# Performance work log

Hardware: AMD Instinct MI355X
Metric: run time of the kernel (lower is better)

The kernel has to match this reference:

```python
import jax, jax.numpy as jnp
import numpy as np

N, K, D = 131072, 64, 256


def setup_inputs() -> dict:
    key = jax.random.key(0)
    k1, k2, k3, k4, k5 = jax.random.split(key, 5)
    X = jax.random.normal(k1, (N, D), dtype=jnp.float32)
    # mixture weights: positive, sum to 1 (log is taken)
    weights = jax.nn.softmax(jax.random.normal(k2, (K,), dtype=jnp.float32))
    means = jax.random.normal(k3, (K, D), dtype=jnp.float32)
    # precision Cholesky factors: lower-triangular with positive diagonal
    tril = jnp.tril(0.01 * jax.random.normal(k4, (K, D, D), dtype=jnp.float32), k=-1)
    diag = 0.5 + jax.random.uniform(k5, (K, D), dtype=jnp.float32)  # in (0.5, 1.5)
    precision_cholesky = tril + jax.vmap(jnp.diag)(diag)
    return {"X": X, "weights": weights, "means": means,
            "precision_cholesky": precision_cholesky}


def reference(X, weights, means, precision_cholesky):
    n_samples, n_features = X.shape
    # log|L_k| = sum of log of diagonal entries (sklearn's strided-diagonal trick)
    log_det = jnp.sum(jnp.log(jnp.diagonal(precision_cholesky, axis1=1, axis2=2)), axis=1)  # (K,)

    # Per-component Mahalanobis distance, sequential over K to avoid an [N,K,D] buffer
    def mahalanobis(args):
        mu, prec_chol = args                      # (D,), (D,D)
        y = X @ prec_chol - mu @ prec_chol        # (N,D)
        return jnp.sum(y * y, axis=1)             # (N,)

    sq = jax.lax.map(mahalanobis, (means, precision_cholesky))  # (K,N)

    log_prob = -0.5 * (n_features * jnp.log(2.0 * jnp.pi) + sq.T) + log_det  # (N,K)
    weighted_log_prob = log_prob + jnp.log(weights)                          # (N,K)
    log_prob_norm = jax.nn.logsumexp(weighted_log_prob, axis=1)              # (N,)
    log_resp = weighted_log_prob - log_prob_norm[:, None]                    # (N,K)
    return jnp.mean(log_prob_norm), log_resp
```

## Files before the change

### kernel.cpp

```cpp
#include <hip/hip_runtime.h>
#include <hip/hip_bf16.h>
#include <cmath>


typedef unsigned short ushort_t;
typedef __attribute__((ext_vector_type(4))) float f32x4;
typedef __attribute__((ext_vector_type(8))) short bf16x8;

constexpr int N_ = 131072;
constexpr int K_ = 64;
constexpr int D_ = 256;
constexpr int BM = 128;
constexpr int NBLK = N_ / BM;
constexpr int SQLD = 68;

__device__ __forceinline__ ushort_t f2bf(float v) {
  unsigned u = __float_as_uint(v);
  u += 0x7FFFu + ((u >> 16) & 1u);
  return (ushort_t)(u >> 16);
}

__device__ __forceinline__ void gld16(const ushort_t* g, ushort_t* l) {
  __builtin_amdgcn_global_load_lds(
      (const __attribute__((address_space(1))) unsigned int*)g,
      (__attribute__((address_space(3))) unsigned int*)l, 16, 0, 0);
}

__device__ __forceinline__ float dpp_red16(float v) {
  int x = __float_as_int(v);
  v += __int_as_float(__builtin_amdgcn_update_dpp(0, x, 0xB1, 0xF, 0xF, true));
  x = __float_as_int(v);
  v += __int_as_float(__builtin_amdgcn_update_dpp(0, x, 0x4E, 0xF, 0xF, true));
  x = __float_as_int(v);
  v += __int_as_float(__builtin_amdgcn_update_dpp(0, x, 0x141, 0xF, 0xF, true));
  x = __float_as_int(v);
  v += __int_as_float(__builtin_amdgcn_update_dpp(0, x, 0x140, 0xF, 0xF, true));
  return v;
}

__global__ void prep_x(const float* __restrict__ X, ushort_t* __restrict__ Xb) {
  for (int e = blockIdx.x * blockDim.x + threadIdx.x; e < N_ * D_;
       e += gridDim.x * blockDim.x) {
    int j = e & 7;
    int lane = (e >> 3) & 63;
    int kc = (e >> 9) & 7;
    int mm = (e >> 12) & 7;
    int T = e >> 15;
    int row = T * 128 + mm * 16 + (lane & 15);
    int col = kc * 32 + (lane >> 4) * 8 + j;
    Xb[e] = f2bf(X[(size_t)row * D_ + col]);
  }
}

__global__ void prep_p(const float* __restrict__ P, ushort_t* __restrict__ Pb) {
  for (int e = blockIdx.x * blockDim.x + threadIdx.x; e < K_ * D_ * D_;
       e += gridDim.x * blockDim.x) {
    int j = e & 7;
    int lane = (e >> 3) & 63;
    int n = (e >> 9) & 3;
    int wc = (e >> 11) & 3;
    int g = e >> 13;
    int k = g >> 3, s = g & 7;
    int row_p = s * 32 + (lane >> 4) * 8 + j;
    int col_p = wc * 64 + n * 16 + (lane & 15);
    Pb[e] = f2bf(P[((size_t)k * D_ + row_p) * D_ + col_p]);
  }
}

__global__ void prep_t(const float* __restrict__ P, const float* __restrict__ mu,
                       const float* __restrict__ w, ushort_t* __restrict__ tvb,
                       float* __restrict__ C) {
  int k = blockIdx.x, j = threadIdx.x;
  const float* Pk = P + (size_t)k * D_ * D_;
  const float* muk = mu + (size_t)k * D_;
  float acc = 0.f;
  for (int i = 0; i < D_; ++i) acc += muk[i] * Pk[(size_t)i * D_ + j];
  tvb[k * D_ + j] = f2bf(acc);
  __shared__ float red[D_];
  red[j] = logf(Pk[(size_t)j * D_ + j]);
  __syncthreads();
  for (int s = 128; s > 0; s >>= 1) {
    if (j < s) red[j] += red[j + s];
    __syncthreads();
  }
  if (j == 0)
    C[k] = red[0] + logf(w[k]) - 0.5f * (float)D_ * logf(2.0f * (float)M_PI);
}

__global__ __launch_bounds__(512, 2) void gmm_main(
    const ushort_t* __restrict__ Xb, const ushort_t* __restrict__ Pb,
    const ushort_t* __restrict__ tvb,
    float* __restrict__ wlp ) {
  __shared__ __align__(16) ushort_t Bl[4][8192];
  __shared__ __align__(16) ushort_t tvl[16384];
  __shared__ float sqf[BM * SQLD];

  const int tid = threadIdx.x;
  const int T = blockIdx.x;
  const int lane = tid & 63, wid = tid >> 6;
  const int wr = wid >> 2, wc = wid & 3;
  const int lc = lane & 15, lg = lane >> 4;

#pragma unroll
  for (int i = 0; i < 17; ++i) sqf[tid + i * 512] = 0.f;

  const ushort_t* Ag = Xb + (size_t)T * 32768;
  bf16x8 Areg[32];
#pragma unroll
  for (int m = 0; m < 4; ++m)
#pragma unroll
    for (int c = 0; c < 8; ++c)
      Areg[m * 8 + c] =
          *(const bf16x8*)&Ag[(((wr * 4 + m) * 8 + c) * 512) + lane * 8];

#pragma unroll
  for (int it = 0; it < 4; ++it)
    gld16(tvb + (it * 512 + tid) * 8, &tvl[(it * 512 + tid) * 8]);
#pragma unroll
  for (int it = 0; it < 2; ++it)
    gld16(Pb + (it * 512 + tid) * 8, &Bl[0][(it * 512 + tid) * 8]);
#pragma unroll
  for (int it = 0; it < 2; ++it)
    gld16(Pb + 8192 + (it * 512 + tid) * 8, &Bl[1][(it * 512 + tid) * 8]);

  asm volatile("s_waitcnt vmcnt(0) lgkmcnt(0)" ::: "memory");
  __builtin_amdgcn_s_barrier();

#pragma unroll 1
  for (int k = 0; k < K_; ++k) {
    f32x4 acc[4][4];
#pragma unroll
    for (int m = 0; m < 4; ++m)
#pragma unroll
      for (int n = 0; n < 4; ++n) acc[m][n] = (f32x4){0.f, 0.f, 0.f, 0.f};

#pragma unroll
    for (int s = 0; s < 8; ++s) {
      const int g2 = k * 8 + s + 2;
      const ushort_t* gb = Pb + (size_t)g2 * 8192;
      ushort_t* db = &Bl[(s + 2) & 3][0];
#pragma unroll
      for (int it = 0; it < 2; ++it)
        gld16(gb + (it * 512 + tid) * 8, db + (it * 512 + tid) * 8);
      asm volatile("s_waitcnt vmcnt(4)" ::: "memory");
      __builtin_amdgcn_s_barrier();

      bf16x8 bb[4];
#pragma unroll
      for (int n = 0; n < 4; ++n)
        bb[n] = *(const bf16x8*)&Bl[s & 3][(wc * 4 + n) * 512 + lane * 8];
#pragma unroll
      for (int m = 0; m < 4; ++m)
#pragma unroll
        for (int n = 0; n < 4; ++n)
          acc[m][n] = __builtin_amdgcn_mfma_f32_16x16x32_bf16(
              Areg[m * 8 + s], bb[n], acc[m][n], 0, 0, 0);
    }

    float tv[4];
#pragma unroll
    for (int n = 0; n < 4; ++n) {
      ushort_t uv = tvl[k * 256 + wc * 64 + n * 16 + lc];
      tv[n] = __uint_as_float((unsigned)uv << 16);
    }
#pragma unroll
    for (int m = 0; m < 4; ++m)
#pragma unroll
      for (int r = 0; r < 4; ++r) {
        float d0 = acc[m][0][r] - tv[0];
        float d1 = acc[m][1][r] - tv[1];
        float d2 = acc[m][2][r] - tv[2];
        float d3 = acc[m][3][r] - tv[3];
        float sfl = dpp_red16(d0 * d0 + d1 * d1 + d2 * d2 + d3 * d3);
        if (lc == 0) {
          int row = wr * 64 + m * 16 + lg * 4 + r;
          atomicAdd(&sqf[row * SQLD + k], sfl);
        }
      }
  }

  __syncthreads();

  float* dst = wlp + (size_t)T * BM * K_;
#pragma unroll
  for (int i = 0; i < 4; ++i) {
    int idx4 = tid + i * 512;
    int row = idx4 >> 4, c4 = idx4 & 15;
    ((f32x4*)dst)[idx4] = *(const f32x4*)&sqf[row * SQLD + c4 * 4];
  }
}

__global__ void lse_k(float* __restrict__ out, const float* __restrict__ C,
                      float* __restrict__ partial) {
  const int row = blockIdx.x * 256 + threadIdx.x;
  float* w = out + 1 + (size_t)row * K_;
  float v[K_];
  float mx = -1e30f;
#pragma unroll
  for (int j = 0; j < K_; ++j) {
    v[j] = -0.5f * w[j] + C[j];
    mx = fmaxf(mx, v[j]);
  }
  float ssum = 0.f;
#pragma unroll
  for (int j = 0; j < K_; ++j) ssum += expf(v[j] - mx);
  float l = mx + logf(ssum);
#pragma unroll
  for (int j = 0; j < K_; ++j) w[j] = v[j] - l;
  __shared__ float red[256];
  red[threadIdx.x] = l;
  __syncthreads();
  for (int s = 128; s > 0; s >>= 1) {
    if (threadIdx.x < s) red[threadIdx.x] += red[threadIdx.x + s];
    __syncthreads();
  }
  if (threadIdx.x == 0) partial[blockIdx.x] = red[0];
}

__global__ void final_red(const float* __restrict__ partial,
                          float* __restrict__ out) {
  __shared__ float red[512];
  red[threadIdx.x] = partial[threadIdx.x];
  __syncthreads();
  for (int s = 256; s > 0; s >>= 1) {
    if (threadIdx.x < s) red[threadIdx.x] += red[threadIdx.x + s];
    __syncthreads();
  }
  if (threadIdx.x == 0) out[0] = red[0] * (1.0f / (float)N_);
}

extern "C" void kernel_launch(void* const* d_in, const int* in_sizes, int n_in,
                              void* d_out, int out_size, void* d_ws,
                              size_t ws_size, hipStream_t stream) {
  const float* X = (const float*)d_in[0];
  const float* w = (const float*)d_in[1];
  const float* mu = (const float*)d_in[2];
  const float* P = (const float*)d_in[3];
  float* out = (float*)d_out;
  char* ws = (char*)d_ws;

  ushort_t* Xb = (ushort_t*)ws;
  ushort_t* Pb = (ushort_t*)(ws + 67108864);
  ushort_t* tvb = (ushort_t*)(ws + 75530240);
  float* C = (float*)(ws + 75563008);
  float* partial = (float*)(ws + 75563264);

  prep_x<<<2048, 256, 0, stream>>>(X, Xb);
  prep_p<<<2048, 256, 0, stream>>>(P, Pb);
  prep_t<<<K_, 256, 0, stream>>>(P, mu, w, tvb, C);
  gmm_main<<<NBLK, 512, 0, stream>>>(Xb, Pb, tvb, out + 1);
  lse_k<<<N_ / 256, 256, 0, stream>>>(out, C, partial);
  final_red<<<1, 512, 0, stream>>>(partial, out);
}
```

Measured before the change: 1.017 ms.

## Switch main GEMM to 32x32x16 MFMA tiles with matching operand layouts

Replaces the 16x16x32 bf16 MFMA tiling with 32x32x16 MFMA instructions. The X and P pre-permutation kernels and the per-wave register layout change to match. The epilogue reduction now covers 32-lane column groups, using a DPP reduction followed by a ds_swizzle across the two 16-lane halves. The intent is higher MFMA throughput and fewer LDS operand reads per FLOP. In exchange, each accumulator is larger and the lane-to-row mapping in the epilogue becomes more complex.

```diff
diff --git a/kernel.cpp b/kernel.cpp
--- a/kernel.cpp
+++ b/kernel.cpp
@@ -4,6 +4,7 @@
 
 
 typedef unsigned short ushort_t;
+typedef __attribute__((ext_vector_type(16))) float f32x16;
 typedef __attribute__((ext_vector_type(4))) float f32x4;
 typedef __attribute__((ext_vector_type(8))) short bf16x8;
 
@@ -42,12 +43,13 @@
   for (int e = blockIdx.x * blockDim.x + threadIdx.x; e < N_ * D_;
        e += gridDim.x * blockDim.x) {
     int j = e & 7;
-    int lane = (e >> 3) & 63;
-    int kc = (e >> 9) & 7;
-    int mm = (e >> 12) & 7;
+    int l = (e >> 3) & 63;
+    int mk = (e >> 9) & 31;
+    int wr = (e >> 14) & 1;
     int T = e >> 15;
-    int row = T * 128 + mm * 16 + (lane & 15);
-    int col = kc * 32 + (lane >> 4) * 8 + j;
+    int mt = mk & 1, ks = mk >> 1;
+    int row = T * 128 + wr * 64 + mt * 32 + (l & 31);
+    int col = ks * 16 + (l >> 5) * 8 + j;
     Xb[e] = f2bf(X[(size_t)row * D_ + col]);
   }
 }
@@ -57,12 +59,13 @@
        e += gridDim.x * blockDim.x) {
     int j = e & 7;
     int lane = (e >> 3) & 63;
-    int n = (e >> 9) & 3;
+    int kc = (e >> 9) & 1;
+    int n = (e >> 10) & 1;
     int wc = (e >> 11) & 3;
     int g = e >> 13;
     int k = g >> 3, s = g & 7;
-    int row_p = s * 32 + (lane >> 4) * 8 + j;
-    int col_p = wc * 64 + n * 16 + (lane & 15);
+    int row_p = s * 32 + kc * 16 + (lane >> 5) * 8 + j;
+    int col_p = wc * 64 + n * 32 + (lane & 31);
     Pb[e] = f2bf(P[((size_t)k * D_ + row_p) * D_ + col_p]);
   }
 }
@@ -99,19 +102,16 @@
   const int T = blockIdx.x;
   const int lane = tid & 63, wid = tid >> 6;
   const int wr = wid >> 2, wc = wid & 3;
-  const int lc = lane & 15, lg = lane >> 4;
+  const int l31 = lane & 31, lh = lane >> 5;
 
 #pragma unroll
   for (int i = 0; i < 17; ++i) sqf[tid + i * 512] = 0.f;
 
-  const ushort_t* Ag = Xb + (size_t)T * 32768;
+  const ushort_t* Ag = Xb + (size_t)(T * 2 + wr) * 16384;
   bf16x8 Areg[32];
 #pragma unroll
-  for (int m = 0; m < 4; ++m)
-#pragma unroll
-    for (int c = 0; c < 8; ++c)
-      Areg[m * 8 + c] =
-          *(const bf16x8*)&Ag[(((wr * 4 + m) * 8 + c) * 512) + lane * 8];
+  for (int f = 0; f < 32; ++f)
+    Areg[f] = *(const bf16x8*)&Ag[f * 512 + lane * 8];
 
 #pragma unroll
   for (int it = 0; it < 4; ++it)
@@ -128,11 +128,20 @@
 
 #pragma unroll 1
   for (int k = 0; k < K_; ++k) {
-    f32x4 acc[4][4];
-#pragma unroll
-    for (int m = 0; m < 4; ++m)
-#pragma unroll
-      for (int n = 0; n < 4; ++n) acc[m][n] = (f32x4){0.f, 0.f, 0.f, 0.f};
+    float tv[2];
+#pragma unroll
+    for (int n = 0; n < 2; ++n) {
+      ushort_t uv = tvl[k * 256 + wc * 64 + n * 32 + l31];
+      tv[n] = __uint_as_float((unsigned)uv << 16);
+    }
+
+    f32x16 acc[2][2];
+#pragma unroll
+    for (int mt = 0; mt < 2; ++mt)
+#pragma unroll
+      for (int n = 0; n < 2; ++n)
+#pragma unroll
+        for (int r = 0; r < 16; ++r) acc[mt][n][r] = 0.f;
 
 #pragma unroll
     for (int s = 0; s < 8; ++s) {
@@ -145,35 +154,34 @@
       asm volatile("s_waitcnt vmcnt(4)" ::: "memory");
       __builtin_amdgcn_s_barrier();
 
-      bf16x8 bb[4];
-#pragma unroll
-      for (int n = 0; n < 4; ++n)
-        bb[n] = *(const bf16x8*)&Bl[s & 3][(wc * 4 + n) * 512 + lane * 8];
-#pragma unroll
-      for (int m = 0; m < 4; ++m)
-#pragma unroll
-        for (int n = 0; n < 4; ++n)
-          acc[m][n] = __builtin_amdgcn_mfma_f32_16x16x32_bf16(
-              Areg[m * 8 + s], bb[n], acc[m][n], 0, 0, 0);
+      bf16x8 bb[2][2];
+#pragma unroll
+      for (int n = 0; n < 2; ++n)
+#pragma unroll
+        for (int kc = 0; kc < 2; ++kc)
+          bb[n][kc] = *(const bf16x8*)&Bl[s & 3]
+                          [((wc * 2 + n) * 2 + kc) * 512 + lane * 8];
+#pragma unroll
+      for (int kc = 0; kc < 2; ++kc)
+#pragma unroll
+        for (int mt = 0; mt < 2; ++mt)
+#pragma unroll
+          for (int n = 0; n < 2; ++n)
+            acc[mt][n] = __builtin_amdgcn_mfma_f32_32x32x16_bf16(
+                Areg[(s * 2 + kc) * 2 + mt], bb[n][kc], acc[mt][n], 0, 0, 0);
     }
 
-    float tv[4];
-#pragma unroll
-    for (int n = 0; n < 4; ++n) {
-      ushort_t uv = tvl[k * 256 + wc * 64 + n * 16 + lc];
-      tv[n] = __uint_as_float((unsigned)uv << 16);
-    }
-#pragma unroll
-    for (int m = 0; m < 4; ++m)
-#pragma unroll
-      for (int r = 0; r < 4; ++r) {
-        float d0 = acc[m][0][r] - tv[0];
-        float d1 = acc[m][1][r] - tv[1];
-        float d2 = acc[m][2][r] - tv[2];
-        float d3 = acc[m][3][r] - tv[3];
-        float sfl = dpp_red16(d0 * d0 + d1 * d1 + d2 * d2 + d3 * d3);
-        if (lc == 0) {
-          int row = wr * 64 + m * 16 + lg * 4 + r;
+#pragma unroll
+    for (int mt = 0; mt < 2; ++mt)
+#pragma unroll
+      for (int r = 0; r < 16; ++r) {
+        float d0 = acc[mt][0][r] - tv[0];
+        float d1 = acc[mt][1][r] - tv[1];
+        float sfl = dpp_red16(d0 * d0 + d1 * d1);
+        sfl += __int_as_float(
+            __builtin_amdgcn_ds_swizzle(__float_as_int(sfl), 0x401F));
+        if (l31 == 0) {
+          int row = wr * 64 + mt * 32 + (r & 3) + 8 * (r >> 2) + 4 * lh;
           atomicAdd(&sqf[row * SQLD + k], sfl);
         }
       }
```

New measurement: 1.482 ms. +45.8%, slower.

## Deepen B-tile prefetch to five LDS buffers and fold mean offset into accumulator init

Applied to the files above, without the earlier changes.

The shared-memory ring for precision-factor tiles grows from four to five buffers and the prefetch distance from two to three stages, with a looser vmcnt wait, so more global loads are in flight during the MFMA loop. The per-component mean projection is loaded before the k-loop body and used as the negated initial accumulator value, which removes the subtractions in the epilogue. MFMA issue is wrapped in raised wave priority. LDS use goes up by one 16 KB buffer, which may reduce occupancy at two blocks per CU, and the clamped tail prefetch issues redundant loads.

```diff
diff --git a/kernel.cpp b/kernel.cpp
--- a/kernel.cpp
+++ b/kernel.cpp
@@ -91,7 +91,7 @@
     const ushort_t* __restrict__ Xb, const ushort_t* __restrict__ Pb,
     const ushort_t* __restrict__ tvb,
     float* __restrict__ wlp ) {
-  __shared__ __align__(16) ushort_t Bl[4][8192];
+  __shared__ __align__(16) ushort_t Bl[5 * 8192];
   __shared__ __align__(16) ushort_t tvl[16384];
   __shared__ float sqf[BM * SQLD];
 
@@ -117,61 +117,71 @@
   for (int it = 0; it < 4; ++it)
     gld16(tvb + (it * 512 + tid) * 8, &tvl[(it * 512 + tid) * 8]);
 #pragma unroll
-  for (int it = 0; it < 2; ++it)
-    gld16(Pb + (it * 512 + tid) * 8, &Bl[0][(it * 512 + tid) * 8]);
-#pragma unroll
-  for (int it = 0; it < 2; ++it)
-    gld16(Pb + 8192 + (it * 512 + tid) * 8, &Bl[1][(it * 512 + tid) * 8]);
+  for (int g0 = 0; g0 < 3; ++g0)
+#pragma unroll
+    for (int it = 0; it < 2; ++it)
+      gld16(Pb + (size_t)g0 * 8192 + (it * 512 + tid) * 8,
+            &Bl[g0 * 8192 + (it * 512 + tid) * 8]);
 
   asm volatile("s_waitcnt vmcnt(0) lgkmcnt(0)" ::: "memory");
   __builtin_amdgcn_s_barrier();
 
+  int bcur = 0;
 #pragma unroll 1
   for (int k = 0; k < K_; ++k) {
+    float tvn[4];
+#pragma unroll
+    for (int n = 0; n < 4; ++n) {
+      ushort_t uv = tvl[k * 256 + wc * 64 + n * 16 + lc];
+      tvn[n] = -__uint_as_float((unsigned)uv << 16);
+    }
     f32x4 acc[4][4];
 #pragma unroll
     for (int m = 0; m < 4; ++m)
 #pragma unroll
-      for (int n = 0; n < 4; ++n) acc[m][n] = (f32x4){0.f, 0.f, 0.f, 0.f};
+      for (int n = 0; n < 4; ++n)
+        acc[m][n] = (f32x4){tvn[n], tvn[n], tvn[n], tvn[n]};
 
 #pragma unroll
     for (int s = 0; s < 8; ++s) {
-      const int g2 = k * 8 + s + 2;
-      const ushort_t* gb = Pb + (size_t)g2 * 8192;
-      ushort_t* db = &Bl[(s + 2) & 3][0];
-#pragma unroll
-      for (int it = 0; it < 2; ++it)
-        gld16(gb + (it * 512 + tid) * 8, db + (it * 512 + tid) * 8);
-      asm volatile("s_waitcnt vmcnt(4)" ::: "memory");
+      {
+        int g3 = k * 8 + s + 3;
+        if (g3 > 511) g3 = 511;
+        int bst = bcur + 3;
+        if (bst >= 5) bst -= 5;
+        const ushort_t* gb = Pb + (size_t)g3 * 8192;
+        ushort_t* db = &Bl[bst * 8192];
+#pragma unroll
+        for (int it = 0; it < 2; ++it)
+          gld16(gb + (it * 512 + tid) * 8, db + (it * 512 + tid) * 8);
+      }
+      asm volatile("s_waitcnt vmcnt(6)" ::: "memory");
       __builtin_amdgcn_s_barrier();
 
       bf16x8 bb[4];
 #pragma unroll
       for (int n = 0; n < 4; ++n)
-        bb[n] = *(const bf16x8*)&Bl[s & 3][(wc * 4 + n) * 512 + lane * 8];
+        bb[n] = *(const bf16x8*)&Bl[bcur * 8192 + (wc * 4 + n) * 512 +
+                                    lane * 8];
+      __builtin_amdgcn_s_setprio(1);
 #pragma unroll
       for (int m = 0; m < 4; ++m)
 #pragma unroll
         for (int n = 0; n < 4; ++n)
           acc[m][n] = __builtin_amdgcn_mfma_f32_16x16x32_bf16(
               Areg[m * 8 + s], bb[n], acc[m][n], 0, 0, 0);
+      __builtin_amdgcn_s_setprio(0);
+
+      bcur = (bcur == 4) ? 0 : bcur + 1;
     }
 
-    float tv[4];
-#pragma unroll
-    for (int n = 0; n < 4; ++n) {
-      ushort_t uv = tvl[k * 256 + wc * 64 + n * 16 + lc];
-      tv[n] = __uint_as_float((unsigned)uv << 16);
-    }
 #pragma unroll
     for (int m = 0; m < 4; ++m)
 #pragma unroll
       for (int r = 0; r < 4; ++r) {
-        float d0 = acc[m][0][r] - tv[0];
-        float d1 = acc[m][1][r] - tv[1];
-        float d2 = acc[m][2][r] - tv[2];
-        float d3 = acc[m][3][r] - tv[3];
-        float sfl = dpp_red16(d0 * d0 + d1 * d1 + d2 * d2 + d3 * d3);
+        float a0 = acc[m][0][r], a1 = acc[m][1][r];
+        float a2 = acc[m][2][r], a3 = acc[m][3][r];
+        float sfl = dpp_red16(a0 * a0 + a1 * a1 + a2 * a2 + a3 * a3);
         if (lc == 0) {
           int row = wr * 64 + m * 16 + lg * 4 + r;
           atomicAdd(&sqf[row * SQLD + k], sfl);
```

New measurement: 1.289 ms. 1.27x slower.
